# Kernel tuning notes

Measured on AMD Instinct MI355X. Metric: run time of the kernel, lower is better.

## Reference

```python
import jax, jax.numpy as jnp
import numpy as np

B, IN, H = 8192, 2048, 2048
EFF = IN + H  # self_recurrent concat of [x_t, state]


def setup_inputs() -> dict:
    key = jax.random.key(0)
    ks = jax.random.split(key, 6)
    s_in = 1.0 / np.sqrt(EFF).astype(np.float32)
    s_h = 1.0 / np.sqrt(H).astype(np.float32)
    return {
        "x_t": jax.random.normal(ks[0], (B, IN), jnp.float32),
        "state": jax.random.normal(ks[1], (B, H), jnp.float32),
        "Wc": jax.random.normal(ks[2], (EFF, H), jnp.float32) * s_in,
        "Uc": jax.random.normal(ks[3], (H, H), jnp.float32) * s_h,
        "bc": jnp.zeros((H,), jnp.float32),
        "Wg": jax.random.normal(ks[4], (EFF, H), jnp.float32) * s_in,
        "Ug": jax.random.normal(ks[5], (H, H), jnp.float32) * s_h,
        "bg": jnp.zeros((H,), jnp.float32),
        "log_step": jnp.zeros((H,), jnp.float32),  # dt_scale=1.0 -> no init shift
        "gamma": jnp.ones((H,), jnp.float32),
        "beta": jnp.zeros((H,), jnp.float32),
    }


def _layernorm(x, gamma, beta, eps=1e-5):
    mu = jnp.mean(x, axis=-1, keepdims=True)
    var = jnp.mean((x - mu) ** 2, axis=-1, keepdims=True)
    return (x - mu) * jax.lax.rsqrt(var + eps) * gamma + beta


def reference(x_t, state, Wc, Uc, bc, Wg, Ug, bg, log_step, gamma, beta):
    dt = 1.0  # step(dt=1.0) * dt_scale(1.0)
    xin = jnp.concatenate([x_t, state], axis=-1)        # [B, EFF], self_recurrent
    cand = jnp.tanh(xin @ Wc + state @ Uc + bc)          # candidate state [B, H]
    gate = jax.nn.sigmoid(xin @ Wg + state @ Ug + bg)    # input gate [B, H]
    tau = jnp.exp(log_step)                              # learned time constant
    alpha = jnp.exp(-dt / tau)                           # exp(-dt/tau) decay
    h_new = alpha * state + (1.0 - alpha) * gate * cand  # liquid gated update
    return _layernorm(h_new, gamma, beta)                # post-norm
```

## Files before the change

kernel.cpp:

```cpp
#include <hip/hip_runtime.h>
#include <hip/hip_bf16.h>
#include <cstdint>
#include <cstddef>

#define Bsz 8192
#define Hdim 2048
#define Kdim 4096
#define Nall 4096

#define BM 256
#define BNH 128
#define BK 64
#define NTILES (Kdim / BK)
#define NITER (NTILES / 2)

typedef __attribute__((ext_vector_type(8))) short short8;
typedef __attribute__((ext_vector_type(4))) short short4v;
typedef __attribute__((ext_vector_type(4))) float floatx4;

__device__ __forceinline__ short f2bf(float f) {
    unsigned u = __float_as_uint(f);
    unsigned r = (u + 0x7fffu + ((u >> 16) & 1u)) >> 16;
    return (short)(r & 0xffffu);
}
__device__ __forceinline__ float bf2f(short s) {
    return __uint_as_float(((unsigned)(unsigned short)s) << 16);
}
__device__ __forceinline__ float fast_tanh(float x) {
    float e = __expf(2.f * x);
    return 1.f - 2.f / (e + 1.f);
}
__device__ __forceinline__ float fast_sigmoid(float x) {
    return 1.f / (1.f + __expf(-x));
}
__device__ __forceinline__ void g2l16(const void* g, void* l) {
    __builtin_amdgcn_global_load_lds(
        (const __attribute__((address_space(1))) unsigned int*)g,
        (__attribute__((address_space(3))) unsigned int*)l,
        16, 0, 0);
}

__global__ __launch_bounds__(256) void build_wt(
    const float* __restrict__ Wc, const float* __restrict__ Uc,
    const float* __restrict__ Wg, const float* __restrict__ Ug,
    short* __restrict__ Wt)
{
    __shared__ float tile[64][257];
    const int nt = blockIdx.x * 64;
    const int kt = blockIdx.y * 256;
    const int tx = threadIdx.x & 15;
    const int ty = threadIdx.x >> 4;
    const bool isGate = (nt >= Hdim);
    const float* W = isGate ? Wg : Wc;
    const float* U = isGate ? Ug : Uc;
    const int ncol = isGate ? (nt - Hdim) : nt;
    const bool useU = (kt >= Hdim);
#pragma unroll 4
    for (int r = 0; r < 256; r += 16) {
        int k = kt + ty + r;
        float4 v = *(const float4*)(W + (size_t)k * Hdim + ncol + tx * 4);
        if (useU) {
            float4 u = *(const float4*)(U + (size_t)(k - Hdim) * Hdim + ncol + tx * 4);
            v.x += u.x; v.y += u.y; v.z += u.z; v.w += u.w;
        }
        int kl = ty + r;
        tile[tx * 4 + 0][kl] = v.x;
        tile[tx * 4 + 1][kl] = v.y;
        tile[tx * 4 + 2][kl] = v.z;
        tile[tx * 4 + 3][kl] = v.w;
    }
    __syncthreads();
    const int n  = threadIdx.x >> 2;
    const int kq = (threadIdx.x & 3) * 64;
    short* dst = Wt + (size_t)(nt + n) * Kdim + kt + kq;
#pragma unroll
    for (int i = 0; i < 8; ++i) {
        short8 o;
#pragma unroll
        for (int e = 0; e < 8; ++e) o[e] = f2bf(tile[n][kq + i * 8 + e]);
        *(short8*)(dst + i * 8) = o;
    }
}

__global__ __launch_bounds__(256) void build_acat(
    const float* __restrict__ x, const float* __restrict__ st,
    short* __restrict__ A)
{
    const int lane = threadIdx.x & 63;
    const int wid = (blockIdx.x * 256 + threadIdx.x) >> 6;
    const size_t base = (size_t)wid * 512;
    const int row = (int)(base >> 12);
    const int c = (int)(base & 4095);
    const float* src = (c < Hdim) ? (x + (size_t)row * Hdim + c)
                                  : (st + (size_t)row * Hdim + (c - Hdim));
    float4 v0 = *(const float4*)(src + lane * 4);
    float4 v1 = *(const float4*)(src + 256 + lane * 4);
    short4v o0, o1;
    o0[0] = f2bf(v0.x); o0[1] = f2bf(v0.y); o0[2] = f2bf(v0.z); o0[3] = f2bf(v0.w);
    o1[0] = f2bf(v1.x); o1[1] = f2bf(v1.y); o1[2] = f2bf(v1.z); o1[3] = f2bf(v1.w);
    short* d = A + base;
    *(short4v*)(d + lane * 4) = o0;
    *(short4v*)(d + 256 + lane * 4) = o1;
}

__device__ __forceinline__ void rdA4(const short* base, const int i0,
                                     short8 (&aF)[4][2],
                                     const int cs0, const int cs1) {
#pragma unroll
    for (int i = 0; i < 4; ++i) {
        aF[i][0] = *(const short8*)(base + (i0 + i) * 16 * BK + cs0);
        aF[i][1] = *(const short8*)(base + (i0 + i) * 16 * BK + cs1);
    }
}
__device__ __forceinline__ void rdB2(const short* base, const int j0,
                                     short8 (&bF)[2][2],
                                     const int cs0, const int cs1) {
#pragma unroll
    for (int j = 0; j < 2; ++j) {
        bF[j][0] = *(const short8*)(base + (j0 + j) * 16 * BK + cs0);
        bF[j][1] = *(const short8*)(base + (j0 + j) * 16 * BK + cs1);
    }
}
__device__ __forceinline__ void mma16(floatx4 (&acc)[8][4], const int ia,
                                      const int jb, const short8 (&aF)[4][2],
                                      const short8 (&bF)[2][2]) {
#pragma unroll
    for (int i = 0; i < 4; ++i)
#pragma unroll
        for (int j = 0; j < 2; ++j) {
            acc[ia + i][jb + j] = __builtin_amdgcn_mfma_f32_16x16x32_bf16(
                aF[i][0], bF[j][0], acc[ia + i][jb + j], 0, 0, 0);
            acc[ia + i][jb + j] = __builtin_amdgcn_mfma_f32_16x16x32_bf16(
                aF[i][1], bF[j][1], acc[ia + i][jb + j], 0, 0, 0);
        }
}

#define STAGE(srcArr, h, dstBase, dstOff, koff) do {               \
    g2l16(srcArr[h][0] + (koff), (dstBase) + dstOff[h][0]);        \
    g2l16(srcArr[h][1] + (koff), (dstBase) + dstOff[h][1]); } while (0)

#define BAR()   __builtin_amdgcn_s_barrier()
#define LGKM0() asm volatile("s_waitcnt lgkmcnt(0)" ::: "memory")
#define VM6()   asm volatile("s_waitcnt vmcnt(6)" ::: "memory")
#define VM0()   asm volatile("s_waitcnt vmcnt(0)" ::: "memory")
#define PRIO1() __builtin_amdgcn_s_setprio(1)
#define PRIO0() __builtin_amdgcn_s_setprio(0)

__global__ __launch_bounds__(512, 2) void gemm_fused(
    const short* __restrict__ A,
    const short* __restrict__ Bt,
    const float* __restrict__ st,
    const float* __restrict__ bc, const float* __restrict__ bg,
    const float* __restrict__ lstep,
    short* __restrict__ Hout)
{
    __shared__ __attribute__((aligned(16))) short lds[4][256 * BK];
    short* const sA0 = &lds[0][0];
    short* const sA1 = &lds[1][0];
    short* const sB0 = &lds[2][0];
    short* const sB1 = &lds[3][0];

    const int tid  = threadIdx.x;
    const int lane = tid & 63;
    const int w    = tid >> 6;
    const int wm = w >> 2;
    const int wn = w & 3;

    const int bid = blockIdx.x;
    const int swz = (bid & 7) * 64 + (bid >> 3);
    const int m0 = (swz >> 4) * BM;
    const int n0 = (swz & 15) * BNH;

    const int r8 = lane >> 3;
    const int c8 = ((lane & 7) ^ r8) * 8;
    const short* aSrc[2][2];
    const short* bSrc[2][2];
    int dstA[2][2], dstB[2][2];
#pragma unroll
    for (int hh = 0; hh < 2; ++hh)
#pragma unroll
        for (int q = 0; q < 2; ++q) {
            int f = w * 2 + q;
            int ra = f * 8 + hh * 64 + (f & 8) * 8;
            int rb = (f >> 2) * 64 + (f & 3) * 8 + hh * 32;
            aSrc[hh][q] = A + (size_t)(m0 + ra + r8) * Kdim + c8;
            int lr = rb + r8;
            int btrow = n0 + ((lr >> 6) << 5) + (lr & 31)
                        + ((lr & 32) ? Hdim : 0);
            bSrc[hh][q] = Bt + (size_t)btrow * Kdim + c8;
            dstA[hh][q] = ra * BK;
            dstB[hh][q] = rb * BK;
        }

    const int fr = lane & 15;
    const int j4 = lane >> 4;
    const int cs0 = ((j4 ^ (fr & 7)) * 8);
    const int cs1 = (((4 + j4) ^ (fr & 7)) * 8);
    const short* A0f = sA0 + (wm * 128 + fr) * BK;
    const short* A1f = sA1 + (wm * 128 + fr) * BK;
    const short* B0f = sB0 + (wn * 64 + fr) * BK;
    const short* B1f = sB1 + (wn * 64 + fr) * BK;

    floatx4 acc[8][4];
#pragma unroll
    for (int i = 0; i < 8; ++i)
#pragma unroll
        for (int j = 0; j < 4; ++j) {
            floatx4 z = {0.f, 0.f, 0.f, 0.f};
            acc[i][j] = z;
        }
    short8 aF[4][2], bLo[2][2], bHi[2][2];

    STAGE(aSrc, 0, sA0, dstA, 0);
    STAGE(aSrc, 1, sA0, dstA, 0);
    STAGE(bSrc, 0, sB0, dstB, 0);
    STAGE(bSrc, 1, sB0, dstB, 0);
    STAGE(aSrc, 0, sA1, dstA, BK);
    STAGE(bSrc, 0, sB1, dstB, BK);
    STAGE(bSrc, 1, sB1, dstB, BK);
    VM6();
    BAR();

    for (int it = 0; it < NITER; ++it) {
        const bool nl = (it < NITER - 1);
        const int k1  = (2 * it + 1) * BK;
        const int k02 = (2 * it + 2) * BK;
        const int k12 = (2 * it + 3) * BK;

        rdA4(A0f, 0, aF, cs0, cs1);
        rdB2(B0f, 0, bLo, cs0, cs1);
        STAGE(aSrc, 1, sA1, dstA, k1);
        BAR(); LGKM0(); PRIO1();
        mma16(acc, 0, 0, aF, bLo);
        PRIO0(); BAR();
        rdB2(B0f, 2, bHi, cs0, cs1);
        if (nl) { STAGE(aSrc, 0, sA0, dstA, k02); }
        BAR(); LGKM0(); PRIO1();
        mma16(acc, 0, 2, aF, bHi);
        PRIO0(); BAR();
        rdA4(A0f, 4, aF, cs0, cs1);
        if (nl) { STAGE(bSrc, 0, sB0, dstB, k02); }
        BAR(); LGKM0(); PRIO1();
        mma16(acc, 4, 0, aF, bLo);
        PRIO0(); BAR();
        if (nl) { STAGE(bSrc, 1, sB0, dstB, k02); VM6(); }
        else    { VM0(); }
        BAR(); PRIO1();
        mma16(acc, 4, 2, aF, bHi);
        PRIO0(); BAR();
        rdA4(A1f, 0, aF, cs0, cs1);
        rdB2(B1f, 0, bLo, cs0, cs1);
        if (nl) { STAGE(aSrc, 1, sA0, dstA, k02); }
        BAR(); LGKM0(); PRIO1();
        mma16(acc, 0, 0, aF, bLo);
        PRIO0(); BAR();
        rdB2(B1f, 2, bHi, cs0, cs1);
        if (nl) { STAGE(aSrc, 0, sA1, dstA, k12); }
        BAR(); LGKM0(); PRIO1();
        mma16(acc, 0, 2, aF, bHi);
        PRIO0(); BAR();
        rdA4(A1f, 4, aF, cs0, cs1);
        if (nl) { STAGE(bSrc, 0, sB1, dstB, k12); }
        BAR(); LGKM0(); PRIO1();
        mma16(acc, 4, 0, aF, bLo);
        PRIO0(); BAR();
        if (nl) { STAGE(bSrc, 1, sB1, dstB, k12); VM6(); }
        BAR(); PRIO1();
        mma16(acc, 4, 2, aF, bHi);
        PRIO0(); BAR();
    }

    __syncthreads();
    float* hv = (float*)&lds[0][0];
    const int cn = lane & 15;
    float bcv[2], bgv[2], alv[2];
#pragma unroll
    for (int j = 0; j < 2; ++j) {
        int col = n0 + wn * 32 + j * 16 + cn;
        bcv[j] = bc[col];
        bgv[j] = bg[col];
        alv[j] = __expf(-__expf(-lstep[col]));
    }
#pragma unroll
    for (int i = 0; i < 8; ++i) {
#pragma unroll
        for (int r = 0; r < 4; ++r) {
            int R = wm * 128 + i * 16 + j4 * 4 + r;
            int swzr = (((R >> 2) & 3) << 4) ^ ((R & 1) << 2);
#pragma unroll
            for (int j = 0; j < 2; ++j) {
                int C = wn * 32 + j * 16 + cn;
                float cand = fast_tanh(acc[i][j][r] + bcv[j]);
                float gate = fast_sigmoid(acc[i][j + 2][r] + bgv[j]);
                hv[R * 128 + (C ^ swzr)] = (1.f - alv[j]) * gate * cand;
            }
        }
    }
    __syncthreads();
    const int co = (tid & 15) * 8;
    const int rw = tid >> 4;
    float al8[8];
#pragma unroll
    for (int e = 0; e < 8; ++e)
        al8[e] = __expf(-__expf(-lstep[n0 + co + e]));
#pragma unroll
    for (int p = 0; p < 8; ++p) {
        int R = p * 32 + rw;
        int row = m0 + R;
        int swzr = (((R >> 2) & 3) << 4) ^ ((R & 1) << 2);
        floatx4 ra = *(const floatx4*)&hv[R * 128 + (co ^ swzr)];
        floatx4 rb = *(const floatx4*)&hv[R * 128 + ((co + 4) ^ swzr)];
        const float* sp = st + (size_t)row * Hdim + n0 + co;
        float4 s0 = *(const float4*)sp;
        float4 s1 = *(const float4*)(sp + 4);
        short8 o;
        o[0] = f2bf(al8[0] * s0.x + ra[0]);
        o[1] = f2bf(al8[1] * s0.y + ra[1]);
        o[2] = f2bf(al8[2] * s0.z + ra[2]);
        o[3] = f2bf(al8[3] * s0.w + ra[3]);
        o[4] = f2bf(al8[4] * s1.x + rb[0]);
        o[5] = f2bf(al8[5] * s1.y + rb[1]);
        o[6] = f2bf(al8[6] * s1.z + rb[2]);
        o[7] = f2bf(al8[7] * s1.w + rb[3]);
        *(short8*)(Hout + (size_t)row * Hdim + n0 + co) = o;
    }
}

__global__ __launch_bounds__(256) void ln_k(
    const short* __restrict__ h, const float* __restrict__ gam,
    const float* __restrict__ bet, float* __restrict__ out)
{
    const int lane = threadIdx.x & 63;
    const int b = blockIdx.x * 4 + (threadIdx.x >> 6);
    const short* hp = h + (size_t)b * Hdim;

    float hv[32];
    float sum = 0.f, ss = 0.f;
#pragma unroll
    for (int q = 0; q < 4; ++q) {
        short8 v = *(const short8*)(hp + q * 512 + lane * 8);
#pragma unroll
        for (int e = 0; e < 8; ++e) {
            float f = bf2f(v[e]);
            hv[q * 8 + e] = f;
            sum += f; ss += f * f;
        }
    }
#pragma unroll
    for (int off = 1; off < 64; off <<= 1) {
        sum += __shfl_xor(sum, off);
        ss  += __shfl_xor(ss, off);
    }
    const float inv = 1.f / (float)Hdim;
    float mu = sum * inv;
    float var = ss * inv - mu * mu;
    float rs = rsqrtf(var + 1e-5f);
    float* op = out + (size_t)b * Hdim;
#pragma unroll
    for (int q = 0; q < 4; ++q) {
#pragma unroll
        for (int hq = 0; hq < 2; ++hq) {
            const int o8 = q * 512 + lane * 8 + hq * 4;
            float4 g  = *(const float4*)(gam + o8);
            float4 be = *(const float4*)(bet + o8);
            float4 o;
            o.x = (hv[q * 8 + hq * 4 + 0] - mu) * rs * g.x + be.x;
            o.y = (hv[q * 8 + hq * 4 + 1] - mu) * rs * g.y + be.y;
            o.z = (hv[q * 8 + hq * 4 + 2] - mu) * rs * g.z + be.z;
            o.w = (hv[q * 8 + hq * 4 + 3] - mu) * rs * g.w + be.w;
            *(float4*)(op + o8) = o;
        }
    }
}

extern "C" void kernel_launch(void* const* d_in, const int* in_sizes, int n_in,
                              void* d_out, int out_size, void* d_ws, size_t ws_size,
                              hipStream_t stream)
{
    const float* x_t   = (const float*)d_in[0];
    const float* state = (const float*)d_in[1];
    const float* Wc    = (const float*)d_in[2];
    const float* Uc    = (const float*)d_in[3];
    const float* bc    = (const float*)d_in[4];
    const float* Wg    = (const float*)d_in[5];
    const float* Ug    = (const float*)d_in[6];
    const float* bg    = (const float*)d_in[7];
    const float* lstep = (const float*)d_in[8];
    const float* gam   = (const float*)d_in[9];
    const float* bet   = (const float*)d_in[10];
    float* out = (float*)d_out;

    char* ws = (char*)d_ws;
    short* Wt   = (short*)ws;
    short* Acat = (short*)(ws + (size_t)32 * 1024 * 1024);
    short* h    = (short*)(ws + (size_t)96 * 1024 * 1024);

    build_wt<<<dim3(Nall / 64, Kdim / 256), 256, 0, stream>>>(Wc, Uc, Wg, Ug, Wt);
    build_acat<<<(Bsz * (Kdim / 8)) / 256, 256, 0, stream>>>(x_t, state, Acat);
    gemm_fused<<<dim3((Bsz / BM) * (Hdim / BNH)), 512, 0, stream>>>(
        Acat, Wt, state, bc, bg, lstep, h);
    ln_k<<<Bsz / 4, 256, 0, stream>>>(h, gam, bet, out);
}
```

Baseline: 499.3 us.

## Merge prep kernels and make GEMM persistent with two tiles per block

Combines the weight-transpose and activation-conversion kernels into one launch, split by block index. The GEMM grid shrinks from 512 to 256 blocks, each looping over two output tiles, so it runs as one persistent wave that fits the CU count. An extra partial LDS wait (lgkmcnt(8)) is added before some barriers. This saves a launch and the tail-wave imbalance, but serialises two tiles per block and drops the overlap that two co-resident blocks per CU could give.

```diff
diff --git a/kernel.cpp b/kernel.cpp
--- a/kernel.cpp
+++ b/kernel.cpp
@@ -40,67 +40,66 @@
         16, 0, 0);
 }
 
-__global__ __launch_bounds__(256) void build_wt(
+__global__ __launch_bounds__(256) void prep_fused(
     const float* __restrict__ Wc, const float* __restrict__ Uc,
     const float* __restrict__ Wg, const float* __restrict__ Ug,
-    short* __restrict__ Wt)
+    const float* __restrict__ x, const float* __restrict__ st,
+    short* __restrict__ Wt, short* __restrict__ Acat)
 {
-    __shared__ float tile[64][257];
-    const int nt = blockIdx.x * 64;
-    const int kt = blockIdx.y * 256;
-    const int tx = threadIdx.x & 15;
-    const int ty = threadIdx.x >> 4;
-    const bool isGate = (nt >= Hdim);
-    const float* W = isGate ? Wg : Wc;
-    const float* U = isGate ? Ug : Uc;
-    const int ncol = isGate ? (nt - Hdim) : nt;
-    const bool useU = (kt >= Hdim);
+    if (blockIdx.x < 1024) {
+        __shared__ float tile[64][257];
+        const int t = blockIdx.x;
+        const int nt = (t & 63) * 64;
+        const int kt = (t >> 6) * 256;
+        const int tx = threadIdx.x & 15;
+        const int ty = threadIdx.x >> 4;
+        const bool isGate = (nt >= Hdim);
+        const float* W = isGate ? Wg : Wc;
+        const float* U = isGate ? Ug : Uc;
+        const int ncol = isGate ? (nt - Hdim) : nt;
+        const bool useU = (kt >= Hdim);
 #pragma unroll 4
-    for (int r = 0; r < 256; r += 16) {
-        int k = kt + ty + r;
-        float4 v = *(const float4*)(W + (size_t)k * Hdim + ncol + tx * 4);
-        if (useU) {
-            float4 u = *(const float4*)(U + (size_t)(k - Hdim) * Hdim + ncol + tx * 4);
-            v.x += u.x; v.y += u.y; v.z += u.z; v.w += u.w;
-        }
-        int kl = ty + r;
-        tile[tx * 4 + 0][kl] = v.x;
-        tile[tx * 4 + 1][kl] = v.y;
-        tile[tx * 4 + 2][kl] = v.z;
-        tile[tx * 4 + 3][kl] = v.w;
-    }
-    __syncthreads();
-    const int n  = threadIdx.x >> 2;
-    const int kq = (threadIdx.x & 3) * 64;
-    short* dst = Wt + (size_t)(nt + n) * Kdim + kt + kq;
-#pragma unroll
-    for (int i = 0; i < 8; ++i) {
-        short8 o;
-#pragma unroll
-        for (int e = 0; e < 8; ++e) o[e] = f2bf(tile[n][kq + i * 8 + e]);
-        *(short8*)(dst + i * 8) = o;
-    }
-}
-
-__global__ __launch_bounds__(256) void build_acat(
-    const float* __restrict__ x, const float* __restrict__ st,
-    short* __restrict__ A)
-{
-    const int lane = threadIdx.x & 63;
-    const int wid = (blockIdx.x * 256 + threadIdx.x) >> 6;
-    const size_t base = (size_t)wid * 512;
-    const int row = (int)(base >> 12);
-    const int c = (int)(base & 4095);
-    const float* src = (c < Hdim) ? (x + (size_t)row * Hdim + c)
-                                  : (st + (size_t)row * Hdim + (c - Hdim));
-    float4 v0 = *(const float4*)(src + lane * 4);
-    float4 v1 = *(const float4*)(src + 256 + lane * 4);
-    short4v o0, o1;
-    o0[0] = f2bf(v0.x); o0[1] = f2bf(v0.y); o0[2] = f2bf(v0.z); o0[3] = f2bf(v0.w);
-    o1[0] = f2bf(v1.x); o1[1] = f2bf(v1.y); o1[2] = f2bf(v1.z); o1[3] = f2bf(v1.w);
-    short* d = A + base;
-    *(short4v*)(d + lane * 4) = o0;
-    *(short4v*)(d + 256 + lane * 4) = o1;
+        for (int r = 0; r < 256; r += 16) {
+            int k = kt + ty + r;
+            float4 v = *(const float4*)(W + (size_t)k * Hdim + ncol + tx * 4);
+            if (useU) {
+                float4 u = *(const float4*)(U + (size_t)(k - Hdim) * Hdim + ncol + tx * 4);
+                v.x += u.x; v.y += u.y; v.z += u.z; v.w += u.w;
+            }
+            int kl = ty + r;
+            tile[tx * 4 + 0][kl] = v.x;
+            tile[tx * 4 + 1][kl] = v.y;
+            tile[tx * 4 + 2][kl] = v.z;
+            tile[tx * 4 + 3][kl] = v.w;
+        }
+        __syncthreads();
+        const int n  = threadIdx.x >> 2;
+        const int kq = (threadIdx.x & 3) * 64;
+        short* dst = Wt + (size_t)(nt + n) * Kdim + kt + kq;
+#pragma unroll
+        for (int i = 0; i < 8; ++i) {
+            short8 o;
+#pragma unroll
+            for (int e = 0; e < 8; ++e) o[e] = f2bf(tile[n][kq + i * 8 + e]);
+            *(short8*)(dst + i * 8) = o;
+        }
+    } else {
+        const int lane = threadIdx.x & 63;
+        const int wid = ((blockIdx.x - 1024) * 256 + threadIdx.x) >> 6;
+        const size_t base = (size_t)wid * 512;
+        const int row = (int)(base >> 12);
+        const int c = (int)(base & 4095);
+        const float* src = (c < Hdim) ? (x + (size_t)row * Hdim + c)
+                                      : (st + (size_t)row * Hdim + (c - Hdim));
+        float4 v0 = *(const float4*)(src + lane * 4);
+        float4 v1 = *(const float4*)(src + 256 + lane * 4);
+        short4v o0, o1;
+        o0[0] = f2bf(v0.x); o0[1] = f2bf(v0.y); o0[2] = f2bf(v0.z); o0[3] = f2bf(v0.w);
+        o1[0] = f2bf(v1.x); o1[1] = f2bf(v1.y); o1[2] = f2bf(v1.z); o1[3] = f2bf(v1.w);
+        short* d = Acat + base;
+        *(short4v*)(d + lane * 4) = o0;
+        *(short4v*)(d + 256 + lane * 4) = o1;
+    }
 }
 
 __device__ __forceinline__ void rdA4(const short* base, const int i0,
@@ -141,6 +140,7 @@
 
 #define BAR()   __builtin_amdgcn_s_barrier()
 #define LGKM0() asm volatile("s_waitcnt lgkmcnt(0)" ::: "memory")
+#define LGKM8() asm volatile("s_waitcnt lgkmcnt(8)" ::: "memory")
 #define VM6()   asm volatile("s_waitcnt vmcnt(6)" ::: "memory")
 #define VM0()   asm volatile("s_waitcnt vmcnt(0)" ::: "memory")
 #define PRIO1() __builtin_amdgcn_s_setprio(1)
@@ -166,16 +166,10 @@
     const int wm = w >> 2;
     const int wn = w & 3;
 
-    const int bid = blockIdx.x;
-    const int swz = (bid & 7) * 64 + (bid >> 3);
-    const int m0 = (swz >> 4) * BM;
-    const int n0 = (swz & 15) * BNH;
-
     const int r8 = lane >> 3;
     const int c8 = ((lane & 7) ^ r8) * 8;
-    const short* aSrc[2][2];
-    const short* bSrc[2][2];
     int dstA[2][2], dstB[2][2];
+    int raOff[2][2], rbRow[2][2];
 #pragma unroll
     for (int hh = 0; hh < 2; ++hh)
 #pragma unroll
@@ -183,11 +177,8 @@
             int f = w * 2 + q;
             int ra = f * 8 + hh * 64 + (f & 8) * 8;
             int rb = (f >> 2) * 64 + (f & 3) * 8 + hh * 32;
-            aSrc[hh][q] = A + (size_t)(m0 + ra + r8) * Kdim + c8;
-            int lr = rb + r8;
-            int btrow = n0 + ((lr >> 6) << 5) + (lr & 31)
-                        + ((lr & 32) ? Hdim : 0);
-            bSrc[hh][q] = Bt + (size_t)btrow * Kdim + c8;
+            raOff[hh][q] = ra;
+            rbRow[hh][q] = rb;
             dstA[hh][q] = ra * BK;
             dstB[hh][q] = rb * BK;
         }
@@ -201,128 +192,154 @@
     const short* B0f = sB0 + (wn * 64 + fr) * BK;
     const short* B1f = sB1 + (wn * 64 + fr) * BK;
 
-    floatx4 acc[8][4];
-#pragma unroll
-    for (int i = 0; i < 8; ++i)
-#pragma unroll
-        for (int j = 0; j < 4; ++j) {
-            floatx4 z = {0.f, 0.f, 0.f, 0.f};
-            acc[i][j] = z;
-        }
     short8 aF[4][2], bLo[2][2], bHi[2][2];
 
-    STAGE(aSrc, 0, sA0, dstA, 0);
-    STAGE(aSrc, 1, sA0, dstA, 0);
-    STAGE(bSrc, 0, sB0, dstB, 0);
-    STAGE(bSrc, 1, sB0, dstB, 0);
-    STAGE(aSrc, 0, sA1, dstA, BK);
-    STAGE(bSrc, 0, sB1, dstB, BK);
-    STAGE(bSrc, 1, sB1, dstB, BK);
-    VM6();
-    BAR();
-
-    for (int it = 0; it < NITER; ++it) {
-        const bool nl = (it < NITER - 1);
-        const int k1  = (2 * it + 1) * BK;
-        const int k02 = (2 * it + 2) * BK;
-        const int k12 = (2 * it + 3) * BK;
-
-        rdA4(A0f, 0, aF, cs0, cs1);
-        rdB2(B0f, 0, bLo, cs0, cs1);
-        STAGE(aSrc, 1, sA1, dstA, k1);
-        BAR(); LGKM0(); PRIO1();
-        mma16(acc, 0, 0, aF, bLo);
-        PRIO0(); BAR();
-        rdB2(B0f, 2, bHi, cs0, cs1);
-        if (nl) { STAGE(aSrc, 0, sA0, dstA, k02); }
-        BAR(); LGKM0(); PRIO1();
-        mma16(acc, 0, 2, aF, bHi);
-        PRIO0(); BAR();
-        rdA4(A0f, 4, aF, cs0, cs1);
-        if (nl) { STAGE(bSrc, 0, sB0, dstB, k02); }
-        BAR(); LGKM0(); PRIO1();
-        mma16(acc, 4, 0, aF, bLo);
-        PRIO0(); BAR();
-        if (nl) { STAGE(bSrc, 1, sB0, dstB, k02); VM6(); }
-        else    { VM0(); }
-        BAR(); PRIO1();
-        mma16(acc, 4, 2, aF, bHi);
-        PRIO0(); BAR();
-        rdA4(A1f, 0, aF, cs0, cs1);
-        rdB2(B1f, 0, bLo, cs0, cs1);
-        if (nl) { STAGE(aSrc, 1, sA0, dstA, k02); }
-        BAR(); LGKM0(); PRIO1();
-        mma16(acc, 0, 0, aF, bLo);
-        PRIO0(); BAR();
-        rdB2(B1f, 2, bHi, cs0, cs1);
-        if (nl) { STAGE(aSrc, 0, sA1, dstA, k12); }
-        BAR(); LGKM0(); PRIO1();
-        mma16(acc, 0, 2, aF, bHi);
-        PRIO0(); BAR();
-        rdA4(A1f, 4, aF, cs0, cs1);
-        if (nl) { STAGE(bSrc, 0, sB1, dstB, k12); }
-        BAR(); LGKM0(); PRIO1();
-        mma16(acc, 4, 0, aF, bLo);
-        PRIO0(); BAR();
-        if (nl) { STAGE(bSrc, 1, sB1, dstB, k12); VM6(); }
-        BAR(); PRIO1();
-        mma16(acc, 4, 2, aF, bHi);
-        PRIO0(); BAR();
-    }
-
-    __syncthreads();
-    float* hv = (float*)&lds[0][0];
-    const int cn = lane & 15;
-    float bcv[2], bgv[2], alv[2];
-#pragma unroll
-    for (int j = 0; j < 2; ++j) {
-        int col = n0 + wn * 32 + j * 16 + cn;
-        bcv[j] = bc[col];
-        bgv[j] = bg[col];
-        alv[j] = __expf(-__expf(-lstep[col]));
-    }
-#pragma unroll
-    for (int i = 0; i < 8; ++i) {
-#pragma unroll
-        for (int r = 0; r < 4; ++r) {
-            int R = wm * 128 + i * 16 + j4 * 4 + r;
+#pragma unroll 1
+    for (int rep = 0; rep < 2; ++rep) {
+        const int vb = blockIdx.x + rep * 256;
+        const int swz = (vb & 7) * 64 + (vb >> 3);
+        const int m0 = (swz >> 4) * BM;
+        const int n0 = (swz & 15) * BNH;
+
+        const short* aSrc[2][2];
+        const short* bSrc[2][2];
+#pragma unroll
+        for (int hh = 0; hh < 2; ++hh)
+#pragma unroll
+            for (int q = 0; q < 2; ++q) {
+                aSrc[hh][q] = A + (size_t)(m0 + raOff[hh][q] + r8) * Kdim + c8;
+                int lr = rbRow[hh][q] + r8;
+                int btrow = n0 + ((lr >> 6) << 5) + (lr & 31)
+                            + ((lr & 32) ? Hdim : 0);
+                bSrc[hh][q] = Bt + (size_t)btrow * Kdim + c8;
+            }
+
+        floatx4 acc[8][4];
+#pragma unroll
+        for (int i = 0; i < 8; ++i)
+#pragma unroll
+            for (int j = 0; j < 4; ++j) {
+                floatx4 z = {0.f, 0.f, 0.f, 0.f};
+                acc[i][j] = z;
+            }
+
+        STAGE(aSrc, 0, sA0, dstA, 0);
+        STAGE(aSrc, 1, sA0, dstA, 0);
+        STAGE(bSrc, 0, sB0, dstB, 0);
+        STAGE(bSrc, 1, sB0, dstB, 0);
+        STAGE(aSrc, 0, sA1, dstA, BK);
+        STAGE(bSrc, 0, sB1, dstB, BK);
+        STAGE(bSrc, 1, sB1, dstB, BK);
+        VM6();
+        BAR();
+
+#pragma unroll 1
+        for (int it = 0; it < NITER; ++it) {
+            const bool nl = (it < NITER - 1);
+            const int k1  = (2 * it + 1) * BK;
+            const int k02 = (2 * it + 2) * BK;
+            const int k12 = (2 * it + 3) * BK;
+
+            rdA4(A0f, 0, aF, cs0, cs1);
+            rdB2(B0f, 0, bLo, cs0, cs1);
+            STAGE(aSrc, 1, sA1, dstA, k1);
+            LGKM8();
+            BAR(); LGKM0(); PRIO1();
+            mma16(acc, 0, 0, aF, bLo);
+            PRIO0(); BAR();
+            rdB2(B0f, 2, bHi, cs0, cs1);
+            if (nl) { STAGE(aSrc, 0, sA0, dstA, k02); }
+            BAR(); LGKM0(); PRIO1();
+            mma16(acc, 0, 2, aF, bHi);
+            PRIO0(); BAR();
+            rdA4(A0f, 4, aF, cs0, cs1);
+            if (nl) { STAGE(bSrc, 0, sB0, dstB, k02); }
+            BAR(); LGKM0(); PRIO1();
+            mma16(acc, 4, 0, aF, bLo);
+            PRIO0(); BAR();
+            if (nl) { STAGE(bSrc, 1, sB0, dstB, k02); VM6(); }
+            else    { VM0(); }
+            BAR(); PRIO1();
+            mma16(acc, 4, 2, aF, bHi);
+            PRIO0(); BAR();
+            rdA4(A1f, 0, aF, cs0, cs1);
+            rdB2(B1f, 0, bLo, cs0, cs1);
+            if (nl) { STAGE(aSrc, 1, sA0, dstA, k02); }
+            LGKM8();
+            BAR(); LGKM0(); PRIO1();
+            mma16(acc, 0, 0, aF, bLo);
+            PRIO0(); BAR();
+            rdB2(B1f, 2, bHi, cs0, cs1);
+            if (nl) { STAGE(aSrc, 0, sA1, dstA, k12); }
+            BAR(); LGKM0(); PRIO1();
+            mma16(acc, 0, 2, aF, bHi);
+            PRIO0(); BAR();
+            rdA4(A1f, 4, aF, cs0, cs1);
+            if (nl) { STAGE(bSrc, 0, sB1, dstB, k12); }
+            BAR(); LGKM0(); PRIO1();
+            mma16(acc, 4, 0, aF, bLo);
+            PRIO0(); BAR();
+            if (nl) { STAGE(bSrc, 1, sB1, dstB, k12); VM6(); }
+            BAR(); PRIO1();
+            mma16(acc, 4, 2, aF, bHi);
+            PRIO0(); BAR();
+        }
+
+        __syncthreads();
+        float* hv = (float*)&lds[0][0];
+        const int cn = lane & 15;
+        float bcv[2], bgv[2], alv[2];
+#pragma unroll
+        for (int j = 0; j < 2; ++j) {
+            int col = n0 + wn * 32 + j * 16 + cn;
+            bcv[j] = bc[col];
+            bgv[j] = bg[col];
+            alv[j] = __expf(-__expf(-lstep[col]));
+        }
+#pragma unroll
+        for (int i = 0; i < 8; ++i) {
+#pragma unroll
+            for (int r = 0; r < 4; ++r) {
+                int R = wm * 128 + i * 16 + j4 * 4 + r;
+                int swzr = (((R >> 2) & 3) << 4) ^ ((R & 1) << 2);
+#pragma unroll
+                for (int j = 0; j < 2; ++j) {
+                    int C = wn * 32 + j * 16 + cn;
+                    float cand = fast_tanh(acc[i][j][r] + bcv[j]);
+                    float gate = fast_sigmoid(acc[i][j + 2][r] + bgv[j]);
+                    hv[R * 128 + (C ^ swzr)] = (1.f - alv[j]) * gate * cand;
+                }
+            }
+        }
+        __syncthreads();
+        const int co = (tid & 15) * 8;
+        const int rw = tid >> 4;
+        float al8[8];
+#pragma unroll
+        for (int e = 0; e < 8; ++e)
+            al8[e] = __expf(-__expf(-lstep[n0 + co + e]));
+#pragma unroll
+        for (int p = 0; p < 8; ++p) {
+            int R = p * 32 + rw;
+            int row = m0 + R;
             int swzr = (((R >> 2) & 3) << 4) ^ ((R & 1) << 2);
-#pragma unroll
-            for (int j = 0; j < 2; ++j) {
-                int C = wn * 32 + j * 16 + cn;
-                float cand = fast_tanh(acc[i][j][r] + bcv[j]);
-                float gate = fast_sigmoid(acc[i][j + 2][r] + bgv[j]);
-                hv[R * 128 + (C ^ swzr)] = (1.f - alv[j]) * gate * cand;
-            }
-        }
-    }
-    __syncthreads();
-    const int co = (tid & 15) * 8;
-    const int rw = tid >> 4;
-    float al8[8];
-#pragma unroll
-    for (int e = 0; e < 8; ++e)
-        al8[e] = __expf(-__expf(-lstep[n0 + co + e]));
-#pragma unroll
-    for (int p = 0; p < 8; ++p) {
-        int R = p * 32 + rw;
-        int row = m0 + R;
-        int swzr = (((R >> 2) & 3) << 4) ^ ((R & 1) << 2);
-        floatx4 ra = *(const floatx4*)&hv[R * 128 + (co ^ swzr)];
-        floatx4 rb = *(const floatx4*)&hv[R * 128 + ((co + 4) ^ swzr)];
-        const float* sp = st + (size_t)row * Hdim + n0 + co;
-        float4 s0 = *(const float4*)sp;
-        float4 s1 = *(const float4*)(sp + 4);
-        short8 o;
-        o[0] = f2bf(al8[0] * s0.x + ra[0]);
-        o[1] = f2bf(al8[1] * s0.y + ra[1]);
-        o[2] = f2bf(al8[2] * s0.z + ra[2]);
-        o[3] = f2bf(al8[3] * s0.w + ra[3]);
-        o[4] = f2bf(al8[4] * s1.x + rb[0]);
-        o[5] = f2bf(al8[5] * s1.y + rb[1]);
-        o[6] = f2bf(al8[6] * s1.z + rb[2]);
-        o[7] = f2bf(al8[7] * s1.w + rb[3]);
-        *(short8*)(Hout + (size_t)row * Hdim + n0 + co) = o;
+            floatx4 ra = *(const floatx4*)&hv[R * 128 + (co ^ swzr)];
+            floatx4 rb = *(const floatx4*)&hv[R * 128 + ((co + 4) ^ swzr)];
+            const float* sp = st + (size_t)row * Hdim + n0 + co;
+            float4 s0 = *(const float4*)sp;
+            float4 s1 = *(const float4*)(sp + 4);
+            short8 o;
+            o[0] = f2bf(al8[0] * s0.x + ra[0]);
+            o[1] = f2bf(al8[1] * s0.y + ra[1]);
+            o[2] = f2bf(al8[2] * s0.z + ra[2]);
+            o[3] = f2bf(al8[3] * s0.w + ra[3]);
+            o[4] = f2bf(al8[4] * s1.x + rb[0]);
+            o[5] = f2bf(al8[5] * s1.y + rb[1]);
+            o[6] = f2bf(al8[6] * s1.z + rb[2]);
+            o[7] = f2bf(al8[7] * s1.w + rb[3]);
+            *(short8*)(Hout + (size_t)row * Hdim + n0 + co) = o;
+        }
+        __syncthreads();
     }
 }
 
@@ -395,9 +412,8 @@
     short* Acat = (short*)(ws + (size_t)32 * 1024 * 1024);
     short* h    = (short*)(ws + (size_t)96 * 1024 * 1024);
 
-    build_wt<<<dim3(Nall / 64, Kdim / 256), 256, 0, stream>>>(Wc, Uc, Wg, Ug, Wt);
-    build_acat<<<(Bsz * (Kdim / 8)) / 256, 256, 0, stream>>>(x_t, state, Acat);
-    gemm_fused<<<dim3((Bsz / BM) * (Hdim / BNH)), 512, 0, stream>>>(
-        Acat, Wt, state, bc, bg, lstep, h);
+    prep_fused<<<1024 + 16384, 256, 0, stream>>>(Wc, Uc, Wg, Ug, x_t, state,
+                                                 Wt, Acat);
+    gemm_fused<<<256, 512, 0, stream>>>(Acat, Wt, state, bc, bg, lstep, h);
     ln_k<<<Bsz / 4, 256, 0, stream>>>(h, gam, bet, out);
 }
```

After: 509.4 us. +2.0%, slower.
